# Kernel optimization log

Measured on AMD Instinct MI355X. Metric: run time of the kernel, lower is better.

Reference implementation:

```python
import jax, jax.numpy as jnp
import numpy as np
import math

B, S, D = 4, 1024, 1024
H, DK = 16, 64
NUM_BUCKETS, MAX_DIST = 32, 128


def _relative_position_bucket(relative_position, num_buckets=NUM_BUCKETS, max_distance=MAX_DIST):
    # bidirectional bucketing (T5 encoder style)
    num_buckets = num_buckets // 2
    buckets = (relative_position > 0).astype(jnp.int32) * num_buckets
    rp = jnp.abs(relative_position)
    max_exact = num_buckets // 2
    is_small = rp < max_exact
    # clamp to >=1 to avoid log(0); masked out by is_small anyway
    rp_large = max_exact + (
        jnp.log(jnp.maximum(rp, 1).astype(jnp.float32) / max_exact)
        / math.log(max_distance / max_exact)
        * (num_buckets - max_exact)
    ).astype(jnp.int32)
    rp_large = jnp.minimum(rp_large, num_buckets - 1)
    return buckets + jnp.where(is_small, rp, rp_large)


def compute_bias(rel_bias_table, q_len, k_len):
    ctx = jnp.arange(q_len)[:, None]
    mem = jnp.arange(k_len)[None, :]
    buckets = _relative_position_bucket(mem - ctx)  # [q,k]
    values = rel_bias_table[buckets]  # [q,k,H]
    return jnp.transpose(values, (2, 0, 1))  # [H,q,k]


def setup_inputs() -> dict:
    key = jax.random.key(0)
    ks = jax.random.split(key, 6)
    return {
        "hidden_states": jax.random.normal(ks[0], (B, S, D), dtype=jnp.float32),
        "Wq": jax.random.normal(ks[1], (D, H * DK), dtype=jnp.float32) * 0.02,
        "Wk": jax.random.normal(ks[2], (D, H * DK), dtype=jnp.float32) * 0.02,
        "Wv": jax.random.normal(ks[3], (D, H * DK), dtype=jnp.float32) * 0.02,
        "Wo": jax.random.normal(ks[4], (H * DK, D), dtype=jnp.float32) * 0.02,
        "rel_bias_table": jax.random.normal(ks[5], (NUM_BUCKETS, H), dtype=jnp.float32),
    }


def reference(hidden_states, Wq, Wk, Wv, Wo, rel_bias_table):
    b, s, _ = hidden_states.shape
    # projections (no bias), split heads -> [b,h,s,dk]
    def heads(x):
        return jnp.transpose(x.reshape(b, s, H, DK), (0, 2, 1, 3))
    q = heads(hidden_states @ Wq)
    k = heads(hidden_states @ Wk)
    v = heads(hidden_states @ Wv)
    # NOTE: T5 attention is UNSCALED (no 1/sqrt(dk))
    scores = jnp.einsum("bhqd,bhkd->bhqk", q, k)
    bias = compute_bias(rel_bias_table, s, s)[None]  # [1,H,s,s]
    scores = scores + bias
    attn = jax.nn.softmax(scores.astype(jnp.float32), axis=-1).astype(scores.dtype)
    out = jnp.einsum("bhqk,bhkd->bhqd", attn, v)
    out = jnp.transpose(out, (0, 2, 1, 3)).reshape(b, s, H * DK)
    return out @ Wo
```

## Files before the change

### kernel.cpp

```cpp
#include <hip/hip_runtime.h>
#include <hip/hip_bf16.h>

typedef __attribute__((ext_vector_type(8))) short short8;
typedef __attribute__((ext_vector_type(4))) float f32x4;
typedef __attribute__((ext_vector_type(4))) unsigned u32x4;
typedef unsigned short u16;

#define AS1 __attribute__((address_space(1)))
#define AS3 __attribute__((address_space(3)))

#define LOG2E 1.44269504088896f
#define FOLD_M 46.166241308446828f
#define EXP2(x) __builtin_amdgcn_exp2f(x)

__device__ __forceinline__ u16 f2bf(float f) {
    unsigned u = __builtin_bit_cast(unsigned, f);
    u += 0x7FFFu + ((u >> 16) & 1u);
    return (u16)(u >> 16);
}

__device__ __forceinline__ unsigned pk2(float a, float b) {
    unsigned ua = __builtin_bit_cast(unsigned, a) + 0x8000u;
    unsigned ub = __builtin_bit_cast(unsigned, b) + 0x8000u;
    return __builtin_amdgcn_perm(ub, ua, 0x07060302);
}

__global__ __launch_bounds__(256) void k_prep(const float* __restrict__ hidden,
                                              const float* __restrict__ Wq, const float* __restrict__ Wk,
                                              const float* __restrict__ Wv, const float* __restrict__ Wo,
                                              const float* __restrict__ tbl,
                                              u16* __restrict__ hidb,
                                              u16* __restrict__ wt, u16* __restrict__ wot,
                                              float* __restrict__ bias2) {
    int z = blockIdx.z;
    if (z >= 5) {
        int i = ((z - 5) * 1024 + blockIdx.y * 32 + blockIdx.x) * 256 + threadIdx.x;
        float4 v = ((const float4*)hidden)[i];
        ushort4 o;
        o.x = f2bf(v.x); o.y = f2bf(v.y); o.z = f2bf(v.z); o.w = f2bf(v.w);
        ((ushort4*)hidb)[i] = o;
        return;
    }
    if (z == 4) {
        int idx = (blockIdx.y * 32 + blockIdx.x) * 256 + threadIdx.x;
        if (idx < 16 * 2048) {
            int r = idx & 2047, h = idx >> 11;
            int rel = r - 1023;
            int bucket = rel > 0 ? 16 : 0;
            int rp = rel < 0 ? -rel : rel;
            if (rp < 8) bucket += rp;
            else {
                int lb = 8 + (int)(log2f((float)rp * 0.125f) * 2.0f);
                bucket += (lb < 15 ? lb : 15);
            }
            bias2[idx] = tbl[bucket * 16 + h] * LOG2E - FOLD_M;
        }
        return;
    }
    const float* in = z == 0 ? Wq : z == 1 ? Wk : z == 2 ? Wv : Wo;
    u16* out = (z == 3) ? wot : wt + (size_t)z * 1024 * 1024;
    __shared__ float tile[32][33];
    int tx = threadIdx.x & 31, ty = threadIdx.x >> 5;
    int bx = blockIdx.x << 5, by = blockIdx.y << 5;
    #pragma unroll
    for (int j = 0; j < 32; j += 8)
        tile[ty + j][tx] = in[(size_t)(by + ty + j) * 1024 + bx + tx];
    __syncthreads();
    #pragma unroll
    for (int j = 0; j < 32; j += 8)
        out[(size_t)(bx + ty + j) * 1024 + by + tx] = f2bf(tile[tx][ty + j]);
}

template<int MODE, int FM>
__global__ __launch_bounds__(256) void k_gemm(const u16* __restrict__ A, const u16* __restrict__ Bt,
                                              u16* __restrict__ oq, u16* __restrict__ ok,
                                              u16* __restrict__ ov, float* __restrict__ outf,
                                              int N) {
    const int K = 1024;
    const int GX = (MODE == 0) ? 24 : 8;
    const int NWG = (MODE == 0) ? 768 : 512;
    __shared__ u16 As[2][FM * 1024];
    __shared__ u16 Bs[2][4096];
    int t = threadIdx.x, lane = t & 63, wave = t >> 6;
    int bid = blockIdx.y * GX + blockIdx.x;
    int sbid = (bid & 7) * (NWG / 8) + (bid >> 3);
    int m0 = (sbid / GX) * (FM * 32), n0 = (sbid % GX) << 7;
    int wm = (wave >> 1) * (FM * 16), wn = (wave & 1) << 6;
    int g = lane >> 4, ln = lane & 15;
    f32x4 acc[FM][4];
    #pragma unroll
    for (int i = 0; i < FM; i++)
        #pragma unroll
        for (int j = 0; j < 4; j++) acc[i][j] = (f32x4){0.f, 0.f, 0.f, 0.f};

    int schunk = ((lane & 3) ^ ((lane >> 3) & 3)) << 3;
    const u16* gA = A + (size_t)(m0 + wave * 16 + (lane >> 2)) * K + schunk;
    const u16* gB = Bt + (size_t)(n0 + wave * 16 + (lane >> 2)) * K + schunk;
    int ldsOff = wave * 512;

    #define GSTAGE(k0_, buf_)                                                                          \
        {                                                                                              \
            __builtin_amdgcn_global_load_lds((const AS1 void*)(gA + (k0_)),                            \
                                             (AS3 void*)&As[buf_][ldsOff], 16, 0, 0);                  \
            if (FM == 4)                                                                               \
                __builtin_amdgcn_global_load_lds((const AS1 void*)(gA + 64 * K + (k0_)),               \
                                                 (AS3 void*)&As[buf_][ldsOff + 2048], 16, 0, 0);       \
            __builtin_amdgcn_global_load_lds((const AS1 void*)(gB + (k0_)),                            \
                                             (AS3 void*)&Bs[buf_][ldsOff], 16, 0, 0);                  \
            __builtin_amdgcn_global_load_lds((const AS1 void*)(gB + 64 * K + (k0_)),                   \
                                             (AS3 void*)&Bs[buf_][ldsOff + 2048], 16, 0, 0);           \
        }

    GSTAGE(0, 0);
    __syncthreads();

    int rchunk = (g ^ ((ln >> 1) & 3)) << 3;

    #pragma unroll 2
    for (int kb = 0; kb < 32; kb++) {
        const int cur = kb & 1;
        if (kb < 31) GSTAGE((kb + 1) * 32, cur ^ 1);

        short8 af[FM], bfr[4];
        #pragma unroll
        for (int fm = 0; fm < FM; fm++)
            af[fm] = *(const short8*)&As[cur][(wm + (fm << 4) + ln) * 32 + rchunk];
        #pragma unroll
        for (int fn = 0; fn < 4; fn++)
            bfr[fn] = *(const short8*)&Bs[cur][(wn + (fn << 4) + ln) * 32 + rchunk];
        #pragma unroll
        for (int fm = 0; fm < FM; fm++)
            #pragma unroll
            for (int fn = 0; fn < 4; fn++)
                acc[fm][fn] = __builtin_amdgcn_mfma_f32_16x16x32_bf16(af[fm], bfr[fn], acc[fm][fn], 0, 0, 0);

        __syncthreads();
    }

    #pragma unroll
    for (int fm = 0; fm < FM; fm++)
        #pragma unroll
        for (int fn = 0; fn < 4; fn++) {
            int mb = m0 + wm + (fm << 4) + (g << 2);
            int n = n0 + wn + (fn << 4) + ln;
            if (MODE == 0) {
                int j = n >> 10, col = n & 1023;
                int h = col >> 6, dk = col & 63;
                int b = mb >> 10, s = mb & 1023;
                if (j == 2) {
                    ushort4 pk;
                    pk.x = f2bf(acc[fm][fn][0]); pk.y = f2bf(acc[fm][fn][1]);
                    pk.z = f2bf(acc[fm][fn][2]); pk.w = f2bf(acc[fm][fn][3]);
                    *(ushort4*)(ov + ((size_t)(((b << 4) + h) * 64 + dk)) * 1024 + s) = pk;
                } else {
                    u16* dst = (j == 0) ? oq : ok;
                    #pragma unroll
                    for (int r = 0; r < 4; r++)
                        dst[((size_t)(((b << 4) + h) * 1024 + s + r)) * 64 + dk] = f2bf(acc[fm][fn][r]);
                }
            } else {
                #pragma unroll
                for (int r = 0; r < 4; r++)
                    outf[(size_t)(mb + r) * N + n] = acc[fm][fn][r];
            }
        }
    #undef GSTAGE
}

__global__ __launch_bounds__(256, 2) void k_attn(const u16* __restrict__ Qg, const u16* __restrict__ Kg,
                                                 const u16* __restrict__ Vtg, const float* __restrict__ bias2,
                                                 u16* __restrict__ attn_out) {
    __shared__ __align__(16) u16 Ks[2][64 * 64];
    __shared__ __align__(16) u16 Vts[2][64 * 64];
    __shared__ __align__(16) float blds4[4][1160];

    int t = threadIdx.x, lane = t & 63, w = t >> 6;
    int bid = blockIdx.x;
    int sid = (bid & 7) * 64 + (bid >> 3);
    int qb = sid & 7, h = (sid >> 3) & 15, b = sid >> 7;
    int q0 = qb << 7;
    const u16* Qh = Qg + ((size_t)(((b << 4) + h) * 1024 + q0)) * 64;
    const u16* Kh = Kg + (size_t)(((b << 4) + h)) * 1024 * 64;
    const u16* Vth = Vtg + (size_t)(((b << 4) + h)) * 64 * 1024;
    const float* bh = bias2 + (h << 11);

    int g = lane >> 4, ln = lane & 15;
    int lnk = (ln & 3) | ((ln & 4) << 1) | ((ln & 8) >> 1);
    int kbq = ((g & 1) << 3) | ((g >> 1) << 2);

    short8 qf[2][2];
    #pragma unroll
    for (int fm = 0; fm < 2; fm++)
        #pragma unroll
        for (int kh = 0; kh < 2; kh++)
            qf[fm][kh] = *(const short8*)(Qh + (size_t)(w * 32 + fm * 16 + ln) * 64 + kh * 32 + g * 8);

    int w0 = 896 - q0;
    for (int i = t; i < 1152; i += 256) {
        float v = bh[w0 + i];
        #pragma unroll
        for (int a2 = 0; a2 < 4; a2++) { int x = i - a2; if (x >= 0) blds4[a2][x] = v; }
    }
    float b_hi = bh[1023 + 256];
    float b_lo = bh[1023 - 256];
    int aRep = (3 - ln) & 3;
    const float* repB = &blds4[aRep][0];

    #define STAGE(kb_, buf_)                                                                     \
        {                                                                                        \
            _Pragma("unroll")                                                                    \
            for (int r2 = 0; r2 < 2; r2++) {                                                     \
                int L = t * 16 + r2 * 4096;                                                      \
                int row = L >> 7, gI = (L >> 4) & 7, gp = gI ^ (row & 7);                        \
                __builtin_amdgcn_global_load_lds(                                                \
                    (const AS1 void*)(Kh + (size_t)((kb_) * 64 + row) * 64 + gp * 8),            \
                    (AS3 void*)&Ks[buf_][L >> 1], 16, 0, 0);                                     \
                __builtin_amdgcn_global_load_lds(                                                \
                    (const AS1 void*)(Vth + (size_t)row * 1024 + (kb_) * 64 + gp * 8),           \
                    (AS3 void*)&Vts[buf_][L >> 1], 16, 0, 0);                                    \
            }                                                                                    \
        }

    STAGE(0, 0);
    __syncthreads();

    float psum[2] = {0.f, 0.f};
    f32x4 o[2][4];
    #pragma unroll
    for (int fm = 0; fm < 2; fm++)
        #pragma unroll
        for (int dn = 0; dn < 4; dn++) o[fm][dn] = (f32x4){0.f, 0.f, 0.f, 0.f};

    #pragma unroll 2
    for (int kb = 0; kb < 16; kb++) {
        const int cur = kb & 1;
        if (kb < 15) STAGE(kb + 1, cur ^ 1);

        f32x4 s[2][4];
        __builtin_amdgcn_s_setprio(1);
        #pragma unroll
        for (int fn = 0; fn < 4; fn++) {
            int row = (fn << 4) + lnk;
            short8 kf0 = *(const short8*)((const char*)Ks[cur] + row * 128 + (((g << 4) + 0)  ^ ((row & 7) << 4)));
            short8 kf1 = *(const short8*)((const char*)Ks[cur] + row * 128 + (((g << 4) + 64) ^ ((row & 7) << 4)));
            #pragma unroll
            for (int fm = 0; fm < 2; fm++) {
                f32x4 a = (f32x4){0.f, 0.f, 0.f, 0.f};
                a = __builtin_amdgcn_mfma_f32_16x16x32_bf16(kf0, qf[fm][0], a, 0, 0, 0);
                a = __builtin_amdgcn_mfma_f32_16x16x32_bf16(kf1, qf[fm][1], a, 0, 0, 0);
                s[fm][fn] = a;
            }
        }
        __builtin_amdgcn_s_setprio(0);

        int d0 = 64 * kb - q0 - 32 * w;
        int ibase = 64 * kb - 32 * w + 127 + kbq - ln;
        bool fast = (d0 >= 122) || (d0 <= -154);
        float bu = d0 > 0 ? b_hi : b_lo;
        unsigned Px[2][4], Py[2][4];
        #pragma unroll
        for (int fm = 0; fm < 2; fm++)
            #pragma unroll
            for (int fn = 0; fn < 4; fn++) {
                f32x4 sv = s[fm][fn];
                float b0, b1, b2v, b3;
                if (fast) { b0 = b1 = b2v = b3 = bu; }
                else {
                    float4 bb = *(const float4*)(repB + (ibase + 16 * fn - 16 * fm - aRep));
                    b0 = bb.x; b1 = bb.y; b2v = bb.z; b3 = bb.w;
                }
                float p0 = EXP2(fmaf(sv[0], LOG2E, b0));
                float p1 = EXP2(fmaf(sv[1], LOG2E, b1));
                float p2 = EXP2(fmaf(sv[2], LOG2E, b2v));
                float p3 = EXP2(fmaf(sv[3], LOG2E, b3));
                psum[fm] += (p0 + p1) + (p2 + p3);
                Px[fm][fn] = pk2(p0, p1);
                Py[fm][fn] = pk2(p2, p3);
            }

        short8 pa[2][2];
        #pragma unroll
        for (int fm = 0; fm < 2; fm++)
            #pragma unroll
            for (int ks = 0; ks < 2; ks++) {
                unsigned w0r = Px[fm][2 * ks], w2r = Px[fm][2 * ks + 1];
                unsigned w1r = Py[fm][2 * ks], w3r = Py[fm][2 * ks + 1];
                asm volatile("s_nop 1\n\tv_permlane32_swap_b32 %0, %1" : "+v"(w0r), "+v"(w2r));
                asm volatile("s_nop 1\n\tv_permlane32_swap_b32 %0, %1" : "+v"(w1r), "+v"(w3r));
                u32x4 tv; tv[0] = w0r; tv[1] = w1r; tv[2] = w2r; tv[3] = w3r;
                pa[fm][ks] = __builtin_bit_cast(short8, tv);
            }

        __builtin_amdgcn_s_setprio(1);
        #pragma unroll
        for (int dn = 0; dn < 4; dn++) {
            int vrow = (dn << 4) + ln;
            short8 vb0 = *(const short8*)((const char*)Vts[cur] + vrow * 128 + (((g << 4) + 0)  ^ ((vrow & 7) << 4)));
            short8 vb1 = *(const short8*)((const char*)Vts[cur] + vrow * 128 + (((g << 4) + 64) ^ ((vrow & 7) << 4)));
            #pragma unroll
            for (int fm = 0; fm < 2; fm++) {
                f32x4 a = o[fm][dn];
                a = __builtin_amdgcn_mfma_f32_16x16x32_bf16(pa[fm][0], vb0, a, 0, 0, 0);
                a = __builtin_amdgcn_mfma_f32_16x16x32_bf16(pa[fm][1], vb1, a, 0, 0, 0);
                o[fm][dn] = a;
            }
        }
        __builtin_amdgcn_s_setprio(0);

        __syncthreads();
    }

    float linv[2][4];
    #pragma unroll
    for (int fm = 0; fm < 2; fm++) {
        float v = psum[fm];
        v += __shfl_xor(v, 16);
        v += __shfl_xor(v, 32);
        float inv = 1.0f / v;
        #pragma unroll
        for (int r = 0; r < 4; r++)
            linv[fm][r] = __shfl(inv, 4 * g + r);
    }
    #pragma unroll
    for (int fm = 0; fm < 2; fm++)
        #pragma unroll
        for (int dn = 0; dn < 4; dn++)
            #pragma unroll
            for (int r = 0; r < 4; r++) {
                int srow = q0 + 32 * w + 16 * fm + (g << 2) + r;
                int col = (h << 6) + (dn << 4) + ln;
                attn_out[((size_t)((b << 10) + srow) << 10) + col] = f2bf(o[fm][dn][r] * linv[fm][r]);
            }
}

extern "C" void kernel_launch(void* const* d_in, const int* in_sizes, int n_in,
                              void* d_out, int out_size, void* d_ws, size_t ws_size,
                              hipStream_t stream) {
    const float* hidden = (const float*)d_in[0];
    const float* Wq = (const float*)d_in[1];
    const float* Wk = (const float*)d_in[2];
    const float* Wv = (const float*)d_in[3];
    const float* Wo = (const float*)d_in[4];
    const float* tbl = (const float*)d_in[5];

    u16* hidb = (u16*)d_ws;
    u16* wt   = hidb + 4096 * 1024;
    u16* wot  = wt + 3072 * 1024;
    u16* Qb   = wot + 1024 * 1024;
    u16* Kb   = Qb + 4 * 16 * 1024 * 64;
    u16* Vb   = Kb + 4 * 16 * 1024 * 64;
    u16* attn = Vb + 4 * 16 * 1024 * 64;
    float* bias = (float*)(attn + 4096 * 1024);

    k_prep<<<dim3(32, 32, 9), 256, 0, stream>>>(hidden, Wq, Wk, Wv, Wo, tbl, hidb, wt, wot, bias);
    k_gemm<0, 4><<<dim3(24, 32), 256, 0, stream>>>(hidb, wt, Qb, Kb, Vb, nullptr, 3072);
    k_attn<<<512, 256, 0, stream>>>(Qb, Kb, Vb, bias, attn);
    k_gemm<1, 2><<<dim3(8, 64), 256, 0, stream>>>(attn, wot, nullptr, nullptr, nullptr,
                                                  (float*)d_out, 1024);
}
```

Measured before the change: 96.79 us.

## Replace QKV projection GEMM with 256x256-tile, 8-wave, swizzled-LDS pipelined kernel

The fused QKV projection now uses a new kernel with 256x256 output tiles, 512 threads (8 waves) and BK=64. Operand tiles are staged through XOR-swizzled LDS and split across four sub-phases with barriers and s_setprio so that global-to-LDS loads overlap MFMA work. The larger tile raises arithmetic intensity and reuse, but the grid shrinks to 192 workgroups on a chip with 256 CUs, and the 128 KB of LDS per block limits occupancy. The output GEMM is split out into its own non-templated kernel with the same logic as before.

```diff
diff --git a/kernel.cpp b/kernel.cpp
--- a/kernel.cpp
+++ b/kernel.cpp
@@ -71,14 +71,124 @@
         out[(size_t)(bx + ty + j) * 1024 + by + tx] = f2bf(tile[tx][ty + j]);
 }
 
-template<int MODE, int FM>
-__global__ __launch_bounds__(256) void k_gemm(const u16* __restrict__ A, const u16* __restrict__ Bt,
-                                              u16* __restrict__ oq, u16* __restrict__ ok,
-                                              u16* __restrict__ ov, float* __restrict__ outf,
-                                              int N) {
-    const int K = 1024;
-    const int GX = (MODE == 0) ? 24 : 8;
-    const int NWG = (MODE == 0) ? 768 : 512;
+__global__ __launch_bounds__(512, 2) void k_gemm256(const u16* __restrict__ A, const u16* __restrict__ Bt,
+                                                    u16* __restrict__ oq, u16* __restrict__ ok,
+                                                    u16* __restrict__ ov) {
+    __shared__ __align__(16) u16 As[2][256 * 64];
+    __shared__ __align__(16) u16 Bs[2][256 * 64];
+    int t = threadIdx.x, lane = t & 63, wave = t >> 6;
+    int g = lane >> 4, ln = lane & 15;
+    int wm2 = wave >> 2, wn4 = wave & 3;
+
+    int bid = blockIdx.y * 12 + blockIdx.x;
+    int sbid = (bid & 7) * 24 + (bid >> 3);
+    int m0 = (sbid / 12) << 8, n0 = (sbid % 12) << 8;
+
+    f32x4 acc[8][4];
+    #pragma unroll
+    for (int i = 0; i < 8; i++)
+        #pragma unroll
+        for (int j = 0; j < 4; j++) acc[i][j] = (f32x4){0.f, 0.f, 0.f, 0.f};
+
+    #define STG_A(kb_, buf_)                                                                     \
+        { _Pragma("unroll")                                                                      \
+          for (int r2 = 0; r2 < 4; r2++) {                                                       \
+              int L = t * 16 + r2 * 8192;                                                        \
+              int row = L >> 7, gI = (L >> 4) & 7, gp = gI ^ (row & 7);                          \
+              __builtin_amdgcn_global_load_lds(                                                  \
+                  (const AS1 void*)(A + (size_t)(m0 + row) * 1024 + (kb_) * 64 + gp * 8),        \
+                  (AS3 void*)&As[buf_][L >> 1], 16, 0, 0); } }
+    #define STG_B(kb_, buf_)                                                                     \
+        { _Pragma("unroll")                                                                      \
+          for (int r2 = 0; r2 < 4; r2++) {                                                       \
+              int L = t * 16 + r2 * 8192;                                                        \
+              int row = L >> 7, gI = (L >> 4) & 7, gp = gI ^ (row & 7);                          \
+              __builtin_amdgcn_global_load_lds(                                                  \
+                  (const AS1 void*)(Bt + (size_t)(n0 + row) * 1024 + (kb_) * 64 + gp * 8),       \
+                  (AS3 void*)&Bs[buf_][L >> 1], 16, 0, 0); } }
+
+    STG_A(0, 0);
+    STG_B(0, 0);
+    asm volatile("s_waitcnt vmcnt(0)" ::: "memory");
+    __syncthreads();
+
+    #pragma unroll 2
+    for (int kb = 0; kb < 16; kb++) {
+        const int c = kb & 1;
+        short8 bfr[4][2];
+        #pragma unroll
+        for (int p = 0; p < 4; p++) {
+            short8 af[2][2];
+            if (p == 0) {
+                #pragma unroll
+                for (int nf = 0; nf < 4; nf++) {
+                    int row = (wn4 << 6) + (nf << 4) + ln;
+                    int sw = (row & 7) << 4;
+                    #pragma unroll
+                    for (int ks = 0; ks < 2; ks++)
+                        bfr[nf][ks] = *(const short8*)((const char*)&Bs[c][0] + row * 128 + (((ks << 6) + (g << 4)) ^ sw));
+                }
+            }
+            #pragma unroll
+            for (int i = 0; i < 2; i++) {
+                int row = (wm2 << 7) + ((2 * p + i) << 4) + ln;
+                int sw = (row & 7) << 4;
+                #pragma unroll
+                for (int ks = 0; ks < 2; ks++)
+                    af[i][ks] = *(const short8*)((const char*)&As[c][0] + row * 128 + (((ks << 6) + (g << 4)) ^ sw));
+            }
+            if (kb < 15) {
+                if (p == 0) STG_A(kb + 1, c ^ 1)
+                else if (p == 1) STG_B(kb + 1, c ^ 1)
+            }
+            if (p == 3) asm volatile("s_waitcnt vmcnt(0)" ::: "memory");
+            __builtin_amdgcn_s_barrier();
+            asm volatile("s_waitcnt lgkmcnt(0)" ::: "memory");
+            __builtin_amdgcn_sched_barrier(0);
+            __builtin_amdgcn_s_setprio(1);
+            #pragma unroll
+            for (int i = 0; i < 2; i++)
+                #pragma unroll
+                for (int nf = 0; nf < 4; nf++) {
+                    f32x4 a = acc[2 * p + i][nf];
+                    a = __builtin_amdgcn_mfma_f32_16x16x32_bf16(af[i][0], bfr[nf][0], a, 0, 0, 0);
+                    a = __builtin_amdgcn_mfma_f32_16x16x32_bf16(af[i][1], bfr[nf][1], a, 0, 0, 0);
+                    acc[2 * p + i][nf] = a;
+                }
+            __builtin_amdgcn_s_setprio(0);
+            __builtin_amdgcn_s_barrier();
+        }
+    }
+    #undef STG_A
+    #undef STG_B
+
+    #pragma unroll
+    for (int mf = 0; mf < 8; mf++)
+        #pragma unroll
+        for (int nf = 0; nf < 4; nf++) {
+            int mb = m0 + (wm2 << 7) + (mf << 4) + (g << 2);
+            int n = n0 + (wn4 << 6) + (nf << 4) + ln;
+            int j = n >> 10, col = n & 1023;
+            int h = col >> 6, dk = col & 63;
+            int b = mb >> 10, s = mb & 1023;
+            if (j == 2) {
+                ushort4 pk;
+                pk.x = f2bf(acc[mf][nf][0]); pk.y = f2bf(acc[mf][nf][1]);
+                pk.z = f2bf(acc[mf][nf][2]); pk.w = f2bf(acc[mf][nf][3]);
+                *(ushort4*)(ov + ((size_t)(((b << 4) + h) * 64 + dk)) * 1024 + s) = pk;
+            } else {
+                u16* dst = (j == 0) ? oq : ok;
+                #pragma unroll
+                for (int r = 0; r < 4; r++)
+                    dst[((size_t)(((b << 4) + h) * 1024 + s + r)) * 64 + dk] = f2bf(acc[mf][nf][r]);
+            }
+        }
+}
+
+__global__ __launch_bounds__(256) void k_gemm_out(const u16* __restrict__ A, const u16* __restrict__ Bt,
+                                                  float* __restrict__ outf) {
+    const int K = 1024, N = 1024, FM = 2;
+    const int GX = 8, NWG = 512;
     __shared__ u16 As[2][FM * 1024];
     __shared__ u16 Bs[2][4096];
     int t = threadIdx.x, lane = t & 63, wave = t >> 6;
@@ -102,9 +212,6 @@
         {                                                                                              \
             __builtin_amdgcn_global_load_lds((const AS1 void*)(gA + (k0_)),                            \
                                              (AS3 void*)&As[buf_][ldsOff], 16, 0, 0);                  \
-            if (FM == 4)                                                                               \
-                __builtin_amdgcn_global_load_lds((const AS1 void*)(gA + 64 * K + (k0_)),               \
-                                                 (AS3 void*)&As[buf_][ldsOff + 2048], 16, 0, 0);       \
             __builtin_amdgcn_global_load_lds((const AS1 void*)(gB + (k0_)),                            \
                                              (AS3 void*)&Bs[buf_][ldsOff], 16, 0, 0);                  \
             __builtin_amdgcn_global_load_lds((const AS1 void*)(gB + 64 * K + (k0_)),                   \
@@ -143,26 +250,9 @@
         for (int fn = 0; fn < 4; fn++) {
             int mb = m0 + wm + (fm << 4) + (g << 2);
             int n = n0 + wn + (fn << 4) + ln;
-            if (MODE == 0) {
-                int j = n >> 10, col = n & 1023;
-                int h = col >> 6, dk = col & 63;
-                int b = mb >> 10, s = mb & 1023;
-                if (j == 2) {
-                    ushort4 pk;
-                    pk.x = f2bf(acc[fm][fn][0]); pk.y = f2bf(acc[fm][fn][1]);
-                    pk.z = f2bf(acc[fm][fn][2]); pk.w = f2bf(acc[fm][fn][3]);
-                    *(ushort4*)(ov + ((size_t)(((b << 4) + h) * 64 + dk)) * 1024 + s) = pk;
-                } else {
-                    u16* dst = (j == 0) ? oq : ok;
-                    #pragma unroll
-                    for (int r = 0; r < 4; r++)
-                        dst[((size_t)(((b << 4) + h) * 1024 + s + r)) * 64 + dk] = f2bf(acc[fm][fn][r]);
-                }
-            } else {
-                #pragma unroll
-                for (int r = 0; r < 4; r++)
-                    outf[(size_t)(mb + r) * N + n] = acc[fm][fn][r];
-            }
+            #pragma unroll
+            for (int r = 0; r < 4; r++)
+                outf[(size_t)(mb + r) * N + n] = acc[fm][fn][r];
         }
     #undef GSTAGE
 }
@@ -353,8 +443,7 @@
     float* bias = (float*)(attn + 4096 * 1024);
 
     k_prep<<<dim3(32, 32, 9), 256, 0, stream>>>(hidden, Wq, Wk, Wv, Wo, tbl, hidb, wt, wot, bias);
-    k_gemm<0, 4><<<dim3(24, 32), 256, 0, stream>>>(hidb, wt, Qb, Kb, Vb, nullptr, 3072);
+    k_gemm256<<<dim3(12, 16), 512, 0, stream>>>(hidb, wt, Qb, Kb, Vb);
     k_attn<<<512, 256, 0, stream>>>(Qb, Kb, Vb, bias, attn);
-    k_gemm<1, 2><<<dim3(8, 64), 256, 0, stream>>>(attn, wot, nullptr, nullptr, nullptr,
-                                                  (float*)d_out, 1024);
-}
+    k_gemm_out<<<dim3(8, 64), 256, 0, stream>>>(attn, wot, (float*)d_out);
+}
```

Result: slower. 99.01 us (+2.3%).

## Triple-buffer GEMM LDS staging with explicit vmcnt waits and MFMA priority

Applied to the files above, without the earlier changes.

Moves the projection/output GEMM mainloop from double buffering to a three-stage LDS ring with two tiles of prefetch in flight. It replaces __syncthreads with explicit s_waitcnt vmcnt counts and raw s_barrier, so only the oldest stage's loads are waited on. It also raises wave priority around the MFMA block. This adds LDS usage, which may reduce occupancy. The hand-counted vmcnt values are fragile if the compiler emits other vector memory ops inside the loop.

```diff
diff --git a/kernel.cpp b/kernel.cpp
--- a/kernel.cpp
+++ b/kernel.cpp
@@ -12,6 +12,7 @@
 #define LOG2E 1.44269504088896f
 #define FOLD_M 46.166241308446828f
 #define EXP2(x) __builtin_amdgcn_exp2f(x)
+#define WAITV(n) asm volatile("s_waitcnt vmcnt(" #n ")" ::: "memory")
 
 __device__ __forceinline__ u16 f2bf(float f) {
     unsigned u = __builtin_bit_cast(unsigned, f);
@@ -79,8 +80,8 @@
     const int K = 1024;
     const int GX = (MODE == 0) ? 24 : 8;
     const int NWG = (MODE == 0) ? 768 : 512;
-    __shared__ u16 As[2][FM * 1024];
-    __shared__ u16 Bs[2][4096];
+    __shared__ __align__(16) u16 As[3][FM * 1024];
+    __shared__ __align__(16) u16 Bs[3][4096];
     int t = threadIdx.x, lane = t & 63, wave = t >> 6;
     int bid = blockIdx.y * GX + blockIdx.x;
     int sbid = (bid & 7) * (NWG / 8) + (bid >> 3);
@@ -100,41 +101,57 @@
 
     #define GSTAGE(k0_, buf_)                                                                          \
         {                                                                                              \
+            u16* sA = &As[buf_][0];                                                                    \
+            u16* sB = &Bs[buf_][0];                                                                    \
             __builtin_amdgcn_global_load_lds((const AS1 void*)(gA + (k0_)),                            \
-                                             (AS3 void*)&As[buf_][ldsOff], 16, 0, 0);                  \
+                                             (AS3 void*)&sA[ldsOff], 16, 0, 0);                        \
             if (FM == 4)                                                                               \
                 __builtin_amdgcn_global_load_lds((const AS1 void*)(gA + 64 * K + (k0_)),               \
-                                                 (AS3 void*)&As[buf_][ldsOff + 2048], 16, 0, 0);       \
+                                                 (AS3 void*)&sA[ldsOff + 2048], 16, 0, 0);             \
             __builtin_amdgcn_global_load_lds((const AS1 void*)(gB + (k0_)),                            \
-                                             (AS3 void*)&Bs[buf_][ldsOff], 16, 0, 0);                  \
+                                             (AS3 void*)&sB[ldsOff], 16, 0, 0);                        \
             __builtin_amdgcn_global_load_lds((const AS1 void*)(gB + 64 * K + (k0_)),                   \
-                                             (AS3 void*)&Bs[buf_][ldsOff + 2048], 16, 0, 0);           \
+                                             (AS3 void*)&sB[ldsOff + 2048], 16, 0, 0);                 \
         }
 
     GSTAGE(0, 0);
-    __syncthreads();
+    GSTAGE(32, 1);
 
     int rchunk = (g ^ ((ln >> 1) & 3)) << 3;
-
-    #pragma unroll 2
+    int c0 = 0, c2 = 2;
+
     for (int kb = 0; kb < 32; kb++) {
-        const int cur = kb & 1;
-        if (kb < 31) GSTAGE((kb + 1) * 32, cur ^ 1);
-
+        if (kb < 30) {
+            GSTAGE((kb + 2) * 32, c2);
+            if (FM == 4) WAITV(8); else WAITV(6);
+        } else if (kb == 30) {
+            if (FM == 4) WAITV(4); else WAITV(3);
+        } else {
+            WAITV(0);
+        }
+        __builtin_amdgcn_s_barrier();
+
+        const u16* rA = &As[c0][0];
+        const u16* rB = &Bs[c0][0];
         short8 af[FM], bfr[4];
         #pragma unroll
         for (int fm = 0; fm < FM; fm++)
-            af[fm] = *(const short8*)&As[cur][(wm + (fm << 4) + ln) * 32 + rchunk];
+            af[fm] = *(const short8*)&rA[(wm + (fm << 4) + ln) * 32 + rchunk];
         #pragma unroll
         for (int fn = 0; fn < 4; fn++)
-            bfr[fn] = *(const short8*)&Bs[cur][(wn + (fn << 4) + ln) * 32 + rchunk];
+            bfr[fn] = *(const short8*)&rB[(wn + (fn << 4) + ln) * 32 + rchunk];
+        __builtin_amdgcn_s_setprio(1);
         #pragma unroll
         for (int fm = 0; fm < FM; fm++)
             #pragma unroll
             for (int fn = 0; fn < 4; fn++)
                 acc[fm][fn] = __builtin_amdgcn_mfma_f32_16x16x32_bf16(af[fm], bfr[fn], acc[fm][fn], 0, 0, 0);
-
-        __syncthreads();
+        __builtin_amdgcn_s_setprio(0);
+        __builtin_amdgcn_s_barrier();
+
+        int old = c0;
+        c0 = (c0 == 2) ? 0 : c0 + 1;
+        c2 = old;
     }
 
     #pragma unroll
```

Measured after the change: 97.24 us. Within noise of the previous version (+0.5%).
